# Kernel optimization log

Hardware: AMD Instinct MI355X
Metric: run time of the kernel (lower is better)

Reference implementation:

```python
import jax, jax.numpy as jnp
import numpy as np

N_NODES = 50000


def gcn_conv(x, row, col, W, b, n_nodes):
    # x: [N, Cin], row/col: [E+N] (self-loops already appended)
    x = x @ W  # [N, Cout]
    deg = jax.ops.segment_sum(jnp.ones(col.shape, x.dtype), col, num_segments=n_nodes)
    dinv = jnp.where(deg > 0, jax.lax.rsqrt(deg), 0.0)
    norm = dinv[row] * dinv[col]  # [E+N]
    msgs = x[row] * norm[:, None]  # gather + scale, [E+N, Cout]
    out = jax.ops.segment_sum(msgs, col, num_segments=n_nodes)
    return out + b


def setup_inputs() -> dict:
    key = jax.random.key(0)
    ks = jax.random.split(key, 5)
    n, e = N_NODES, 640000
    d_in, d_h, d_out = 128, 128, 64
    x = jax.random.normal(ks[0], (n, d_in), dtype=jnp.float32)
    edge_index = jax.random.randint(ks[1], (2, e), 0, n, dtype=jnp.int64)
    s1 = 1.0 / np.sqrt(d_in)
    s2 = 1.0 / np.sqrt(d_h)
    W1 = jax.random.normal(ks[2], (d_in, d_h), dtype=jnp.float32) * s1
    W2 = jax.random.normal(ks[3], (d_h, d_h), dtype=jnp.float32) * s2
    Wl = jax.random.normal(ks[4], (d_h, d_out), dtype=jnp.float32) * s2
    return {
        "x": x, "edge_index": edge_index,
        "W1": W1, "b1": jnp.zeros((d_h,), jnp.float32),
        "W2": W2, "b2": jnp.zeros((d_h,), jnp.float32),
        "Wl": Wl, "bl": jnp.zeros((d_out,), jnp.float32),
    }


def reference(x, edge_index, W1, b1, W2, b2, Wl, bl):
    n = x.shape[0]
    loops = jnp.arange(n, dtype=edge_index.dtype)
    row = jnp.concatenate([edge_index[0], loops])  # add self-loops (PyG GCNConv)
    col = jnp.concatenate([edge_index[1], loops])
    h = jax.nn.relu(gcn_conv(x, row, col, W1, b1, n))  # dropout is identity in eval
    h = jax.nn.relu(gcn_conv(h, row, col, W2, b2, n))
    return h @ Wl + bl
```

## Files before the change

### kernel.cpp

```cpp
#include <hip/hip_runtime.h>

#define NN 50000
#define NE 640000
#define RB ((NN + 255) / 256)

struct __align__(8) edge_t { int r; float w; };

__global__ void k_detect(const unsigned* __restrict__ w, int* __restrict__ flag) {
    __shared__ int found;
    if (threadIdx.x == 0) found = 0;
    __syncthreads();
    int j = threadIdx.x * 2499;
    if (w[2 * j + 1] != 0u) atomicAdd(&found, 1);
    __syncthreads();
    if (threadIdx.x == 0) *flag = (found == 0) ? 1 : 0;
}

__device__ __forceinline__ int edge_at(const void* p, long long i, int m64) {
    if (m64) return (int)((const long long*)p)[i];
    return ((const int*)p)[i];
}

__global__ void k_count(const void* __restrict__ e, const int* __restrict__ flag,
                        int* __restrict__ deg) {
    int i = blockIdx.x * 256 + threadIdx.x;
    if (i >= NE) return;
    int m = *flag;
    int c = edge_at(e, (long long)NE + i, m);
    if ((unsigned)c < (unsigned)NN) atomicAdd(&deg[c], 1);
}

__global__ __launch_bounds__(256) void k_reduce(const int* __restrict__ deg,
                                                int* __restrict__ bsum) {
    __shared__ int s[256];
    int i = blockIdx.x * 256 + threadIdx.x;
    s[threadIdx.x] = (i < NN) ? deg[i] : 0;
    __syncthreads();
    for (int d = 128; d > 0; d >>= 1) {
        if (threadIdx.x < d) s[threadIdx.x] += s[threadIdx.x + d];
        __syncthreads();
    }
    if (threadIdx.x == 0) bsum[blockIdx.x] = s[0];
}

__global__ __launch_bounds__(256) void k_scanb(const int* __restrict__ bsum,
                                               int* __restrict__ bpref) {
    __shared__ int s[256];
    int t = threadIdx.x;
    s[t] = (t < RB) ? bsum[t] : 0;
    __syncthreads();
    for (int d = 1; d < 256; d <<= 1) {
        int v = (t >= d) ? s[t - d] : 0;
        __syncthreads();
        s[t] += v;
        __syncthreads();
    }
    if (t < RB) bpref[t] = (t == 0) ? 0 : s[t - 1];
}

__global__ __launch_bounds__(256) void k_apply(const int* __restrict__ deg,
                                               const int* __restrict__ bpref,
                                               int* __restrict__ offs,
                                               int* __restrict__ cursor,
                                               float* __restrict__ dinv) {
    __shared__ int s[256];
    int t = threadIdx.x;
    int i = blockIdx.x * 256 + t;
    int dg = (i < NN) ? deg[i] : 0;
    s[t] = dg;
    __syncthreads();
    for (int d = 1; d < 256; d <<= 1) {
        int v = (t >= d) ? s[t - d] : 0;
        __syncthreads();
        s[t] += v;
        __syncthreads();
    }
    if (i < NN) {
        int excl = bpref[blockIdx.x] + s[t] - dg;
        offs[i] = excl;
        cursor[i] = excl;
        dinv[i] = rsqrtf((float)(dg + 1));
        if (i == NN - 1) offs[NN] = excl + dg;
    }
}

__global__ void k_scatter(const void* __restrict__ e, const int* __restrict__ flag,
                          int* __restrict__ cursor, edge_t* __restrict__ ew,
                          const float* __restrict__ dinv) {
    int i = blockIdx.x * 256 + threadIdx.x;
    if (i >= NE) return;
    int m = *flag;
    int c = edge_at(e, (long long)NE + i, m);
    if ((unsigned)c >= (unsigned)NN) return;
    int r = edge_at(e, (long long)i, m);
    r = min(max(r, 0), NN - 1);
    int p = atomicAdd(&cursor[c], 1);
    edge_t t2; t2.r = r; t2.w = dinv[r];
    ew[p] = t2;
}

__global__ __launch_bounds__(256) void k_gemm128(const float* __restrict__ A,
                                                 const float* __restrict__ W,
                                                 float* __restrict__ T) {
    __shared__ float Ws[128 * 128];
    int t = threadIdx.x;
#pragma unroll
    for (int i = 0; i < 16; i++)
        ((float4*)Ws)[t + 256 * i] = ((const float4*)W)[t + 256 * i];
    __syncthreads();
    int rg = t >> 4, cg = t & 15;
    int row0 = blockIdx.x * 64 + rg * 4;
    const float* a0 = A + (long long)min(row0 + 0, NN - 1) * 128;
    const float* a1 = A + (long long)min(row0 + 1, NN - 1) * 128;
    const float* a2 = A + (long long)min(row0 + 2, NN - 1) * 128;
    const float* a3 = A + (long long)min(row0 + 3, NN - 1) * 128;
    float acc[4][8];
#pragma unroll
    for (int i = 0; i < 4; i++)
#pragma unroll
        for (int j = 0; j < 8; j++) acc[i][j] = 0.f;
#pragma unroll 8
    for (int k = 0; k < 128; k++) {
        float4 w0 = *(const float4*)&Ws[k * 128 + cg * 4];
        float4 w1 = *(const float4*)&Ws[k * 128 + cg * 4 + 64];
        float a[4] = {a0[k], a1[k], a2[k], a3[k]};
#pragma unroll
        for (int i = 0; i < 4; i++) {
            acc[i][0] += a[i] * w0.x; acc[i][1] += a[i] * w0.y;
            acc[i][2] += a[i] * w0.z; acc[i][3] += a[i] * w0.w;
            acc[i][4] += a[i] * w1.x; acc[i][5] += a[i] * w1.y;
            acc[i][6] += a[i] * w1.z; acc[i][7] += a[i] * w1.w;
        }
    }
#pragma unroll
    for (int i = 0; i < 4; i++) {
        int row = row0 + i;
        if (row < NN) {
            float4 v0 = {acc[i][0], acc[i][1], acc[i][2], acc[i][3]};
            float4 v1 = {acc[i][4], acc[i][5], acc[i][6], acc[i][7]};
            *(float4*)&T[(long long)row * 128 + cg * 4] = v0;
            *(float4*)&T[(long long)row * 128 + cg * 4 + 64] = v1;
        }
    }
}

__global__ __launch_bounds__(256) void k_gemm64(const float* __restrict__ A,
                                                const float* __restrict__ W,
                                                const float* __restrict__ b,
                                                float* __restrict__ T) {
    __shared__ float Ws[128 * 64];
    int t = threadIdx.x;
#pragma unroll
    for (int i = 0; i < 8; i++)
        ((float4*)Ws)[t + 256 * i] = ((const float4*)W)[t + 256 * i];
    __syncthreads();
    int rg = t >> 4, cg = t & 15;
    int row0 = blockIdx.x * 64 + rg * 4;
    const float* a0 = A + (long long)min(row0 + 0, NN - 1) * 128;
    const float* a1 = A + (long long)min(row0 + 1, NN - 1) * 128;
    const float* a2 = A + (long long)min(row0 + 2, NN - 1) * 128;
    const float* a3 = A + (long long)min(row0 + 3, NN - 1) * 128;
    float acc[4][4];
#pragma unroll
    for (int i = 0; i < 4; i++)
#pragma unroll
        for (int j = 0; j < 4; j++) acc[i][j] = 0.f;
#pragma unroll 8
    for (int k = 0; k < 128; k++) {
        float4 w = *(const float4*)&Ws[k * 64 + cg * 4];
        float a[4] = {a0[k], a1[k], a2[k], a3[k]};
#pragma unroll
        for (int i = 0; i < 4; i++) {
            acc[i][0] += a[i] * w.x; acc[i][1] += a[i] * w.y;
            acc[i][2] += a[i] * w.z; acc[i][3] += a[i] * w.w;
        }
    }
    float4 bb = ((const float4*)b)[cg];
#pragma unroll
    for (int i = 0; i < 4; i++) {
        int row = row0 + i;
        if (row < NN) {
            float4 v = {acc[i][0] + bb.x, acc[i][1] + bb.y,
                        acc[i][2] + bb.z, acc[i][3] + bb.w};
            *(float4*)&T[(long long)row * 64 + cg * 4] = v;
        }
    }
}

__global__ __launch_bounds__(256) void k_agg(const float* __restrict__ X,
                                             const int* __restrict__ offs,
                                             const edge_t* __restrict__ ew,
                                             const float* __restrict__ dinv,
                                             const float* __restrict__ b,
                                             float* __restrict__ H) {
    int t = threadIdx.x;
    int node = blockIdx.x * 4 + (t >> 6);
    int h = t & 63;
    if (node >= NN) return;
    const float2* X2 = (const float2*)X;
    float dc = dinv[node];
    float2 self = X2[(long long)node * 64 + h];
    float accx = dc * self.x, accy = dc * self.y;
    int e0 = offs[node], e1 = offs[node + 1];
    const edge_t* ep = ew + e0;
    int n = e1 - e0;
    int i = 0;
    for (; i + 8 <= n; i += 8) {
        edge_t m0 = ep[i+0], m1 = ep[i+1], m2 = ep[i+2], m3 = ep[i+3];
        edge_t m4 = ep[i+4], m5 = ep[i+5], m6 = ep[i+6], m7 = ep[i+7];
        float2 v0 = X2[(long long)m0.r * 64 + h];
        float2 v1 = X2[(long long)m1.r * 64 + h];
        float2 v2 = X2[(long long)m2.r * 64 + h];
        float2 v3 = X2[(long long)m3.r * 64 + h];
        float2 v4 = X2[(long long)m4.r * 64 + h];
        float2 v5 = X2[(long long)m5.r * 64 + h];
        float2 v6 = X2[(long long)m6.r * 64 + h];
        float2 v7 = X2[(long long)m7.r * 64 + h];
        accx += m0.w * v0.x + m1.w * v1.x + m2.w * v2.x + m3.w * v3.x
              + m4.w * v4.x + m5.w * v5.x + m6.w * v6.x + m7.w * v7.x;
        accy += m0.w * v0.y + m1.w * v1.y + m2.w * v2.y + m3.w * v3.y
              + m4.w * v4.y + m5.w * v5.y + m6.w * v6.y + m7.w * v7.y;
    }
    for (; i + 4 <= n; i += 4) {
        edge_t m0 = ep[i+0], m1 = ep[i+1], m2 = ep[i+2], m3 = ep[i+3];
        float2 v0 = X2[(long long)m0.r * 64 + h];
        float2 v1 = X2[(long long)m1.r * 64 + h];
        float2 v2 = X2[(long long)m2.r * 64 + h];
        float2 v3 = X2[(long long)m3.r * 64 + h];
        accx += m0.w * v0.x + m1.w * v1.x + m2.w * v2.x + m3.w * v3.x;
        accy += m0.w * v0.y + m1.w * v1.y + m2.w * v2.y + m3.w * v3.y;
    }
    for (; i < n; i++) {
        edge_t m = ep[i];
        float2 v = X2[(long long)m.r * 64 + h];
        accx += m.w * v.x;
        accy += m.w * v.y;
    }
    float2 bb = ((const float2*)b)[h];
    float2 o;
    o.x = fmaxf(dc * accx + bb.x, 0.f);
    o.y = fmaxf(dc * accy + bb.y, 0.f);
    *(float2*)&H[(long long)node * 128 + 2 * h] = o;
}

extern "C" void kernel_launch(void* const* d_in, const int* in_sizes, int n_in,
                              void* d_out, int out_size, void* d_ws, size_t ws_size,
                              hipStream_t stream) {
    const float* x  = (const float*)d_in[0];
    const void*  ei = d_in[1];
    const float* W1 = (const float*)d_in[2];
    const float* b1 = (const float*)d_in[3];
    const float* W2 = (const float*)d_in[4];
    const float* b2 = (const float*)d_in[5];
    const float* Wl = (const float*)d_in[6];
    const float* bl = (const float*)d_in[7];
    float* out = (float*)d_out;

    char* ws = (char*)d_ws;
    size_t off = 0;
    auto alloc = [&](size_t bytes) {
        void* p = ws + off;
        off += (bytes + 255) & ~(size_t)255;
        return p;
    };
    float*  t0     = (float*)alloc((size_t)NN * 128 * 4);
    float*  t1     = (float*)alloc((size_t)NN * 128 * 4);
    int*    deg    = (int*)alloc((size_t)NN * 4);
    int*    offs   = (int*)alloc((size_t)(NN + 1) * 4);
    int*    cursor = (int*)alloc((size_t)NN * 4);
    edge_t* ewbuf  = (edge_t*)alloc((size_t)NE * 8);
    float*  dinv   = (float*)alloc((size_t)NN * 4);
    int*    bsum   = (int*)alloc((size_t)RB * 4);
    int*    bpref  = (int*)alloc((size_t)RB * 4);
    int*    flag   = (int*)alloc(256);

    hipMemsetAsync(deg, 0, (size_t)NN * 4, stream);
    k_detect<<<1, 256, 0, stream>>>((const unsigned*)ei, flag);
    k_count<<<(NE + 255) / 256, 256, 0, stream>>>(ei, flag, deg);
    k_reduce<<<RB, 256, 0, stream>>>(deg, bsum);
    k_scanb<<<1, 256, 0, stream>>>(bsum, bpref);
    k_apply<<<RB, 256, 0, stream>>>(deg, bpref, offs, cursor, dinv);
    k_scatter<<<(NE + 255) / 256, 256, 0, stream>>>(ei, flag, cursor, ewbuf, dinv);

    int gb = (NN + 63) / 64;
    k_gemm128<<<gb, 256, 0, stream>>>(x, W1, t0);
    k_agg<<<(NN + 3) / 4, 256, 0, stream>>>(t0, offs, ewbuf, dinv, b1, t1);
    k_gemm128<<<gb, 256, 0, stream>>>(t1, W2, t0);
    k_agg<<<(NN + 3) / 4, 256, 0, stream>>>(t0, offs, ewbuf, dinv, b2, t1);
    k_gemm64<<<gb, 256, 0, stream>>>(t1, Wl, bl, out);
}
```

Before: 333.8 us.

## Enlarge GEMM row tile to 8 rows per thread and split agg edges across half-waves

The GEMM kernels now compute 8 rows per thread (128 rows per block) instead of 4, so each shared-memory weight load is reused across more rows. This raises register pressure and halves the number of blocks. The aggregation kernel now has each 64-lane wave cover a node with two 32-lane halves. Each half handles alternate edges and does float4 gathers, and the halves are combined with a cross-half shuffle. This gives wider memory transactions and more edges in flight per node, but half the lanes sit idle at the store.

```diff
diff --git a/kernel.cpp b/kernel.cpp
--- a/kernel.cpp
+++ b/kernel.cpp
@@ -109,23 +109,27 @@
         ((float4*)Ws)[t + 256 * i] = ((const float4*)W)[t + 256 * i];
     __syncthreads();
     int rg = t >> 4, cg = t & 15;
-    int row0 = blockIdx.x * 64 + rg * 4;
+    int row0 = blockIdx.x * 128 + rg * 8;
     const float* a0 = A + (long long)min(row0 + 0, NN - 1) * 128;
     const float* a1 = A + (long long)min(row0 + 1, NN - 1) * 128;
     const float* a2 = A + (long long)min(row0 + 2, NN - 1) * 128;
     const float* a3 = A + (long long)min(row0 + 3, NN - 1) * 128;
-    float acc[4][8];
-#pragma unroll
-    for (int i = 0; i < 4; i++)
+    const float* a4 = A + (long long)min(row0 + 4, NN - 1) * 128;
+    const float* a5 = A + (long long)min(row0 + 5, NN - 1) * 128;
+    const float* a6 = A + (long long)min(row0 + 6, NN - 1) * 128;
+    const float* a7 = A + (long long)min(row0 + 7, NN - 1) * 128;
+    float acc[8][8];
+#pragma unroll
+    for (int i = 0; i < 8; i++)
 #pragma unroll
         for (int j = 0; j < 8; j++) acc[i][j] = 0.f;
-#pragma unroll 8
+#pragma unroll 2
     for (int k = 0; k < 128; k++) {
         float4 w0 = *(const float4*)&Ws[k * 128 + cg * 4];
         float4 w1 = *(const float4*)&Ws[k * 128 + cg * 4 + 64];
-        float a[4] = {a0[k], a1[k], a2[k], a3[k]};
-#pragma unroll
-        for (int i = 0; i < 4; i++) {
+        float a[8] = {a0[k], a1[k], a2[k], a3[k], a4[k], a5[k], a6[k], a7[k]};
+#pragma unroll
+        for (int i = 0; i < 8; i++) {
             acc[i][0] += a[i] * w0.x; acc[i][1] += a[i] * w0.y;
             acc[i][2] += a[i] * w0.z; acc[i][3] += a[i] * w0.w;
             acc[i][4] += a[i] * w1.x; acc[i][5] += a[i] * w1.y;
@@ -133,7 +137,7 @@
         }
     }
 #pragma unroll
-    for (int i = 0; i < 4; i++) {
+    for (int i = 0; i < 8; i++) {
         int row = row0 + i;
         if (row < NN) {
             float4 v0 = {acc[i][0], acc[i][1], acc[i][2], acc[i][3]};
@@ -155,29 +159,33 @@
         ((float4*)Ws)[t + 256 * i] = ((const float4*)W)[t + 256 * i];
     __syncthreads();
     int rg = t >> 4, cg = t & 15;
-    int row0 = blockIdx.x * 64 + rg * 4;
+    int row0 = blockIdx.x * 128 + rg * 8;
     const float* a0 = A + (long long)min(row0 + 0, NN - 1) * 128;
     const float* a1 = A + (long long)min(row0 + 1, NN - 1) * 128;
     const float* a2 = A + (long long)min(row0 + 2, NN - 1) * 128;
     const float* a3 = A + (long long)min(row0 + 3, NN - 1) * 128;
-    float acc[4][4];
-#pragma unroll
-    for (int i = 0; i < 4; i++)
+    const float* a4 = A + (long long)min(row0 + 4, NN - 1) * 128;
+    const float* a5 = A + (long long)min(row0 + 5, NN - 1) * 128;
+    const float* a6 = A + (long long)min(row0 + 6, NN - 1) * 128;
+    const float* a7 = A + (long long)min(row0 + 7, NN - 1) * 128;
+    float acc[8][4];
+#pragma unroll
+    for (int i = 0; i < 8; i++)
 #pragma unroll
         for (int j = 0; j < 4; j++) acc[i][j] = 0.f;
-#pragma unroll 8
+#pragma unroll 2
     for (int k = 0; k < 128; k++) {
         float4 w = *(const float4*)&Ws[k * 64 + cg * 4];
-        float a[4] = {a0[k], a1[k], a2[k], a3[k]};
-#pragma unroll
-        for (int i = 0; i < 4; i++) {
+        float a[8] = {a0[k], a1[k], a2[k], a3[k], a4[k], a5[k], a6[k], a7[k]};
+#pragma unroll
+        for (int i = 0; i < 8; i++) {
             acc[i][0] += a[i] * w.x; acc[i][1] += a[i] * w.y;
             acc[i][2] += a[i] * w.z; acc[i][3] += a[i] * w.w;
         }
     }
     float4 bb = ((const float4*)b)[cg];
 #pragma unroll
-    for (int i = 0; i < 4; i++) {
+    for (int i = 0; i < 8; i++) {
         int row = row0 + i;
         if (row < NN) {
             float4 v = {acc[i][0] + bb.x, acc[i][1] + bb.y,
@@ -195,52 +203,51 @@
                                              float* __restrict__ H) {
     int t = threadIdx.x;
     int node = blockIdx.x * 4 + (t >> 6);
-    int h = t & 63;
     if (node >= NN) return;
-    const float2* X2 = (const float2*)X;
+    int lane = t & 63;
+    int half = lane >> 5;
+    int l32 = lane & 31;
+    const float4* X4 = (const float4*)X;
     float dc = dinv[node];
-    float2 self = X2[(long long)node * 64 + h];
-    float accx = dc * self.x, accy = dc * self.y;
+    float4 acc = {0.f, 0.f, 0.f, 0.f};
+    if (half == 0) {
+        float4 s = X4[(long long)node * 32 + l32];
+        acc.x = dc * s.x; acc.y = dc * s.y; acc.z = dc * s.z; acc.w = dc * s.w;
+    }
     int e0 = offs[node], e1 = offs[node + 1];
+    int n = e1 - e0;
     const edge_t* ep = ew + e0;
-    int n = e1 - e0;
-    int i = 0;
-    for (; i + 8 <= n; i += 8) {
-        edge_t m0 = ep[i+0], m1 = ep[i+1], m2 = ep[i+2], m3 = ep[i+3];
-        edge_t m4 = ep[i+4], m5 = ep[i+5], m6 = ep[i+6], m7 = ep[i+7];
-        float2 v0 = X2[(long long)m0.r * 64 + h];
-        float2 v1 = X2[(long long)m1.r * 64 + h];
-        float2 v2 = X2[(long long)m2.r * 64 + h];
-        float2 v3 = X2[(long long)m3.r * 64 + h];
-        float2 v4 = X2[(long long)m4.r * 64 + h];
-        float2 v5 = X2[(long long)m5.r * 64 + h];
-        float2 v6 = X2[(long long)m6.r * 64 + h];
-        float2 v7 = X2[(long long)m7.r * 64 + h];
-        accx += m0.w * v0.x + m1.w * v1.x + m2.w * v2.x + m3.w * v3.x
-              + m4.w * v4.x + m5.w * v5.x + m6.w * v6.x + m7.w * v7.x;
-        accy += m0.w * v0.y + m1.w * v1.y + m2.w * v2.y + m3.w * v3.y
-              + m4.w * v4.y + m5.w * v5.y + m6.w * v6.y + m7.w * v7.y;
-    }
-    for (; i + 4 <= n; i += 4) {
-        edge_t m0 = ep[i+0], m1 = ep[i+1], m2 = ep[i+2], m3 = ep[i+3];
-        float2 v0 = X2[(long long)m0.r * 64 + h];
-        float2 v1 = X2[(long long)m1.r * 64 + h];
-        float2 v2 = X2[(long long)m2.r * 64 + h];
-        float2 v3 = X2[(long long)m3.r * 64 + h];
-        accx += m0.w * v0.x + m1.w * v1.x + m2.w * v2.x + m3.w * v3.x;
-        accy += m0.w * v0.y + m1.w * v1.y + m2.w * v2.y + m3.w * v3.y;
-    }
-    for (; i < n; i++) {
+    int i = half;
+    for (; i + 6 < n; i += 8) {
+        edge_t m0 = ep[i], m1 = ep[i + 2], m2 = ep[i + 4], m3 = ep[i + 6];
+        float4 v0 = X4[(long long)m0.r * 32 + l32];
+        float4 v1 = X4[(long long)m1.r * 32 + l32];
+        float4 v2 = X4[(long long)m2.r * 32 + l32];
+        float4 v3 = X4[(long long)m3.r * 32 + l32];
+        acc.x += m0.w * v0.x + m1.w * v1.x + m2.w * v2.x + m3.w * v3.x;
+        acc.y += m0.w * v0.y + m1.w * v1.y + m2.w * v2.y + m3.w * v3.y;
+        acc.z += m0.w * v0.z + m1.w * v1.z + m2.w * v2.z + m3.w * v3.z;
+        acc.w += m0.w * v0.w + m1.w * v1.w + m2.w * v2.w + m3.w * v3.w;
+    }
+    for (; i < n; i += 2) {
         edge_t m = ep[i];
-        float2 v = X2[(long long)m.r * 64 + h];
-        accx += m.w * v.x;
-        accy += m.w * v.y;
-    }
-    float2 bb = ((const float2*)b)[h];
-    float2 o;
-    o.x = fmaxf(dc * accx + bb.x, 0.f);
-    o.y = fmaxf(dc * accy + bb.y, 0.f);
-    *(float2*)&H[(long long)node * 128 + 2 * h] = o;
+        float4 v = X4[(long long)m.r * 32 + l32];
+        acc.x += m.w * v.x; acc.y += m.w * v.y;
+        acc.z += m.w * v.z; acc.w += m.w * v.w;
+    }
+    float4 oth;
+    oth.x = __shfl_xor(acc.x, 32);
+    oth.y = __shfl_xor(acc.y, 32);
+    oth.z = __shfl_xor(acc.z, 32);
+    oth.w = __shfl_xor(acc.w, 32);
+    float4 bb = ((const float4*)b)[l32];
+    float4 o;
+    o.x = fmaxf(dc * (acc.x + oth.x) + bb.x, 0.f);
+    o.y = fmaxf(dc * (acc.y + oth.y) + bb.y, 0.f);
+    o.z = fmaxf(dc * (acc.z + oth.z) + bb.z, 0.f);
+    o.w = fmaxf(dc * (acc.w + oth.w) + bb.w, 0.f);
+    if (half == 0)
+        ((float4*)H)[(long long)node * 32 + l32] = o;
 }
 
 extern "C" void kernel_launch(void* const* d_in, const int* in_sizes, int n_in,
@@ -282,7 +289,7 @@
     k_apply<<<RB, 256, 0, stream>>>(deg, bpref, offs, cursor, dinv);
     k_scatter<<<(NE + 255) / 256, 256, 0, stream>>>(ei, flag, cursor, ewbuf, dinv);
 
-    int gb = (NN + 63) / 64;
+    int gb = (NN + 127) / 128;
     k_gemm128<<<gb, 256, 0, stream>>>(x, W1, t0);
     k_agg<<<(NN + 3) / 4, 256, 0, stream>>>(t0, offs, ewbuf, dinv, b1, t1);
     k_gemm128<<<gb, 256, 0, stream>>>(t1, W2, t0);
```

New measurement: 358.0 us. 7.3% more time.
